# Optimization experiments

Measured on AMD Instinct MI355X. Metric: run time of the kernel, lower is better.

Reference implementation:

```python
import jax, jax.numpy as jnp
import numpy as np

NEG_SLOPE = 0.01  # torch F.leaky_relu default
NUM_USER, NUM_ITEM, DIM = 50000, 30000, 64
N_NODES = NUM_USER + NUM_ITEM
N_INTER = 800000
N_LAYERS = 2


def _leaky(x):
    return jax.nn.leaky_relu(x, NEG_SLOPE)


def _gcn_tower(features, preference, id_embedding, W, b, row, col):
    # x = cat(preference, features); F.normalize (L2 per row)
    x = jnp.concatenate([preference, features], axis=0)  # [N, 64]
    x = x / jnp.maximum(jnp.linalg.norm(x, axis=1, keepdims=True), 1e-12)
    deg = jax.ops.segment_sum(jnp.ones(row.shape, x.dtype), row, num_segments=N_NODES)  # bincount(row)
    for i in range(N_LAYERS):
        # Abstract_GCN: scatter-mean of gathered neighbor feats, then linear
        agg = jax.ops.segment_sum(x[col], row, num_segments=N_NODES) / deg[:, None]
        h = _leaky(agg @ W[i, 0].T + b[i, 0])
        # has_id=True, concate=False
        x_hat = _leaky(x @ W[i, 1].T + b[i, 1]) + id_embedding
        x = _leaky(h @ W[i, 2].T + b[i, 2] + x_hat)
    return x


def setup_inputs() -> dict:
    key = jax.random.key(0)
    ks = jax.random.split(key, 14)
    # bipartite user->item edges with full node coverage (every node appears
    # as a row after symmetrization, matching real interaction data where
    # bincount(row) has no zeros)
    r1 = jnp.arange(NUM_USER, dtype=jnp.int64 if jax.config.jax_enable_x64 else jnp.int32)
    c1 = jax.random.randint(ks[0], (NUM_USER,), NUM_USER, N_NODES)
    r2 = jax.random.randint(ks[1], (NUM_ITEM,), 0, NUM_USER)
    c2 = NUM_USER + jnp.arange(NUM_ITEM, dtype=r1.dtype)
    rest = N_INTER - NUM_USER - NUM_ITEM
    r3 = jax.random.randint(ks[2], (rest,), 0, NUM_USER)
    c3 = jax.random.randint(ks[3], (rest,), NUM_USER, N_NODES)
    row0 = jnp.concatenate([r1, r2, r3])
    col0 = jnp.concatenate([c1, c2, c3])
    # symmetrize: cat(edge_index, edge_index[[1,0]])
    edge_index = jnp.stack([jnp.concatenate([row0, col0]),
                            jnp.concatenate([col0, row0])])  # [2, 1.6M]
    s = 0.1  # xavier-ish scale for 64x64
    return {
        "v_feat": jax.random.normal(ks[4], (NUM_ITEM, DIM), jnp.float32),
        "t_feat": jax.random.normal(ks[5], (NUM_ITEM, DIM), jnp.float32),
        "id_embedding": jax.random.normal(ks[6], (N_NODES, DIM), jnp.float32) * s,
        "v_pref": jax.random.normal(ks[7], (NUM_USER, DIM), jnp.float32) * s,
        "t_pref": jax.random.normal(ks[8], (NUM_USER, DIM), jnp.float32) * s,
        "v_W": jax.random.normal(ks[9], (N_LAYERS, 3, DIM, DIM), jnp.float32) * s,
        "v_b": jnp.zeros((N_LAYERS, 3, DIM), jnp.float32),
        "t_W": jax.random.normal(ks[10], (N_LAYERS, 3, DIM, DIM), jnp.float32) * s,
        "t_b": jnp.zeros((N_LAYERS, 3, DIM), jnp.float32),
        "edge_index": edge_index,
    }


def reference(v_feat, t_feat, id_embedding, v_pref, t_pref, v_W, v_b, t_W, t_b, edge_index):
    row, col = edge_index[0], edge_index[1]
    rep_v = _gcn_tower(v_feat, v_pref, id_embedding, v_W, v_b, row, col)
    rep_t = _gcn_tower(t_feat, t_pref, id_embedding, t_W, t_b, row, col)
    return (rep_v + rep_t) / 2.0  # MMGCN.get_rep representation
```

## Files before the change

### kernel.cpp

```cpp
#include <hip/hip_runtime.h>
#include <hip/hip_bf16.h>

#define NUM_USER 50000
#define N_NODES  80000
#define DIM      64
#define NEG_SLOPE 0.01f

#define NB 313
#define BSHIFT 8
#define RMASK 255
#define CSHIFT 17
#define CMASK 0x1FFFF
#define CAP 10240

typedef __attribute__((ext_vector_type(8))) short short8;
typedef __attribute__((ext_vector_type(4))) float f32x4;

typedef unsigned short XT;

__device__ __forceinline__ float leaky(float v) {
    return v > 0.0f ? v : v * NEG_SLOPE;
}

__device__ __forceinline__ int load_idx(const void* ei, int is64, long long pos) {
    if (is64) return (int)((const long long*)ei)[pos];
    return ((const int*)ei)[pos];
}
__device__ __forceinline__ float load_f(const void* p, int isbf16, size_t i) {
    if (isbf16) return __bfloat162float(((const __hip_bfloat16*)p)[i]);
    return ((const float*)p)[i];
}

__device__ __forceinline__ unsigned short f2bf(float f) {
    unsigned u = __float_as_uint(f);
    u += 0x7fffu + ((u >> 16) & 1u);
    return (unsigned short)(u >> 16);
}

__device__ __forceinline__ void acc8(float* a, uint4 r) {
    a[0] += __uint_as_float(r.x << 16);
    a[1] += __uint_as_float(r.x & 0xffff0000u);
    a[2] += __uint_as_float(r.y << 16);
    a[3] += __uint_as_float(r.y & 0xffff0000u);
    a[4] += __uint_as_float(r.z << 16);
    a[5] += __uint_as_float(r.z & 0xffff0000u);
    a[6] += __uint_as_float(r.w << 16);
    a[7] += __uint_as_float(r.w & 0xffff0000u);
}

__global__ void detect_kernel(const unsigned int* __restrict__ feat_words,
                              const int* __restrict__ ei_words,
                              int* __restrict__ flags,
                              int* __restrict__ bucketCur) {
    int lane = threadIdx.x & 63;
    for (int i = lane; i < 320; i += 64) bucketCur[i] = 0;
    int orv = 0;
    for (int i = lane * 2 + 1; i < 1024; i += 128) orv |= ei_words[i];
    int hits = 0;
    for (int i = lane; i < 256; i += 64) {
        unsigned e = (feat_words[i] >> 7) & 0xFF;
        hits += (e == 126 || e == 127) ? 1 : 0;
    }
    #pragma unroll
    for (int d = 32; d > 0; d >>= 1) {
        orv  |= __shfl_xor(orv, d, 64);
        hits += __shfl_xor(hits, d, 64);
    }
    if (lane == 0 && blockIdx.x == 0) {
        flags[0] = (orv == 0) ? 1 : 0;
        flags[1] = (hits > 64) ? 1 : 0;
    }
}

__global__ __launch_bounds__(256) void megafuse_kernel(
        const void* __restrict__ ei, int E, int binBlocks, int initBlocks,
        const int* __restrict__ flags,
        int* __restrict__ bucketCur, unsigned int* __restrict__ recs,
        const void* __restrict__ vp, const void* __restrict__ tp,
        const void* __restrict__ vf, const void* __restrict__ tf,
        XT* __restrict__ xc,
        const void* __restrict__ vW, const void* __restrict__ tW,
        const void* __restrict__ vb, const void* __restrict__ tb,
        unsigned short* __restrict__ Wbf, float* __restrict__ bfp) {
    if ((int)blockIdx.x < binBlocks) {
        __shared__ int bloc[320];
        __shared__ int bres[320];
        int tid = threadIdx.x;
        for (int i = tid; i < 320; i += 256) bloc[i] = 0;
        __syncthreads();
        int is64 = flags[0];
        long long base = (long long)blockIdx.x * 2048;
        int bb[8], cc[8], lp[8], rl[8];
        #pragma unroll
        for (int it = 0; it < 8; ++it) {
            bb[it] = -1;
            long long e = base + it * 256 + tid;
            if (e < E) {
                int r = load_idx(ei, is64, e);
                int c = load_idx(ei, is64, (long long)E + e);
                if ((unsigned)r < N_NODES && (unsigned)c < N_NODES) {
                    int b = r >> BSHIFT;
                    bb[it] = b;
                    cc[it] = c;
                    rl[it] = r & RMASK;
                    lp[it] = atomicAdd(&bloc[b], 1);
                }
            }
        }
        __syncthreads();
        for (int i = tid; i < NB; i += 256) {
            int v = bloc[i];
            bres[i] = v ? atomicAdd(&bucketCur[i], v) : 0;
        }
        __syncthreads();
        #pragma unroll
        for (int it = 0; it < 8; ++it) {
            if (bb[it] >= 0) {
                int pos = bres[bb[it]] + lp[it];
                if (pos < CAP)
                    recs[(size_t)bb[it] * CAP + pos] =
                        ((unsigned)rl[it] << CSHIFT) | (unsigned)cc[it];
            }
        }
    } else if ((int)blockIdx.x < binBlocks + initBlocks) {
        int n = (blockIdx.x - binBlocks) * 4 + (threadIdx.x >> 6);
        if (n >= N_NODES) return;
        int lane = threadIdx.x & 63;
        int isb = flags[1];
        float a, b;
        if (n < NUM_USER) {
            a = load_f(vp, isb, (size_t)n * DIM + lane);
            b = load_f(tp, isb, (size_t)n * DIM + lane);
        } else {
            a = load_f(vf, isb, (size_t)(n - NUM_USER) * DIM + lane);
            b = load_f(tf, isb, (size_t)(n - NUM_USER) * DIM + lane);
        }
        float sa = a * a, sb = b * b;
        #pragma unroll
        for (int d = 32; d > 0; d >>= 1) {
            sa += __shfl_xor(sa, d, 64);
            sb += __shfl_xor(sb, d, 64);
        }
        float ra = 1.0f / fmaxf(sqrtf(sa), 1e-12f);
        float rb = 1.0f / fmaxf(sqrtf(sb), 1e-12f);
        xc[(size_t)n * 128 + lane]      = f2bf(a * ra);
        xc[(size_t)n * 128 + 64 + lane] = f2bf(b * rb);
    } else {
        int isb = flags[1];
        int j = (blockIdx.x - binBlocks - initBlocks) * 256 + threadIdx.x;
        if (j < 2 * 24576) {
            int tw = j / 24576, r = j % 24576;
            Wbf[j] = f2bf(load_f(tw ? tW : vW, isb, r));
        } else if (j < 2 * 24576 + 2 * 384) {
            int i2 = j - 2 * 24576;
            int tw = i2 / 384, r = i2 % 384;
            bfp[i2] = load_f(tw ? tb : vb, isb, r);
        }
    }
}

__global__ __launch_bounds__(1024) void bin2csr_kernel(
        const unsigned int* __restrict__ recs,
        const int* __restrict__ bucketCur,
        int* __restrict__ cnt, int* __restrict__ cur,
        int* __restrict__ csr) {
    __shared__ int rcnt[256];
    __shared__ int sc[256];
    __shared__ int lcur[256];
    int b = blockIdx.x;
    int t = threadIdx.x;
    int base = b * CAP;
    int count = bucketCur[b];
    if (count > CAP) count = CAP;

    if (t < 256) { rcnt[t] = 0; lcur[t] = 0; }
    __syncthreads();
    for (int i = t; i < count; i += 1024) {
        unsigned rec = recs[(size_t)base + i];
        atomicAdd(&rcnt[rec >> CSHIFT], 1);
    }
    __syncthreads();
    int v = (t < 256) ? rcnt[t] : 0;
    if (t < 256) sc[t] = v;
    __syncthreads();
    for (int d = 1; d < 256; d <<= 1) {
        int x = 0;
        if (t < 256) { x = sc[t]; if (t >= d) x += sc[t - d]; }
        __syncthreads();
        if (t < 256) sc[t] = x;
        __syncthreads();
    }
    if (t < 256) {
        int row = (b << BSHIFT) + t;
        if (row < N_NODES) {
            cnt[row] = v;
            cur[row] = base + sc[t];
        }
    }
    __syncthreads();
    for (int i = t; i < count; i += 1024) {
        unsigned rec = recs[(size_t)base + i];
        int rloc = rec >> CSHIFT;
        int c = rec & CMASK;
        int pos = base + (sc[rloc] - rcnt[rloc]) + atomicAdd(&lcur[rloc], 1);
        csr[pos] = c;
    }
}

__global__ __launch_bounds__(512) void gather_kernel(
        const XT* __restrict__ xc, XT* __restrict__ agg,
        const int* __restrict__ cnt, const int* __restrict__ cur,
        const int* __restrict__ csr) {
    int n = blockIdx.x * 8 + (threadIdx.x >> 6);
    if (n >= N_NODES) return;
    int lane = threadIdx.x & 63;
    int g8 = lane >> 3;
    int s  = lane & 7;
    int gg = g8 >> 1;
    int h  = g8 & 1;

    int d = cnt[n];
    int base = cur[n] - d;
    const int* nb = csr + base;
    const XT* xh = xc + h * 64;

    float acc[8];
    #pragma unroll
    for (int f = 0; f < 8; ++f) acc[f] = 0.f;

    int jj = gg;
    for (; jj + 4 < d; jj += 8) {
        int c0 = nb[jj];
        int c1 = nb[jj + 4];
        uint4 r0 = ((const uint4*)(xh + (size_t)c0 * 128))[s];
        uint4 r1 = ((const uint4*)(xh + (size_t)c1 * 128))[s];
        acc8(acc, r0);
        acc8(acc, r1);
    }
    if (jj < d) {
        int c0 = nb[jj];
        uint4 r0 = ((const uint4*)(xh + (size_t)c0 * 128))[s];
        acc8(acc, r0);
    }

    #pragma unroll
    for (int dd = 16; dd < 64; dd <<= 1) {
        #pragma unroll
        for (int f = 0; f < 8; ++f) acc[f] += __shfl_xor(acc[f], dd, 64);
    }

    float invd = (d > 0) ? 1.0f / (float)d : 0.0f;
    if (g8 < 2) {
        uint4 w;
        w.x = (unsigned)f2bf(acc[0] * invd) | ((unsigned)f2bf(acc[1] * invd) << 16);
        w.y = (unsigned)f2bf(acc[2] * invd) | ((unsigned)f2bf(acc[3] * invd) << 16);
        w.z = (unsigned)f2bf(acc[4] * invd) | ((unsigned)f2bf(acc[5] * invd) << 16);
        w.w = (unsigned)f2bf(acc[6] * invd) | ((unsigned)f2bf(acc[7] * invd) << 16);
        ((uint4*)(agg + (size_t)n * 128 + h * 64))[s] = w;
    }
}

__global__ __launch_bounds__(256) void dense_mfma_kernel(
        XT* __restrict__ xc, const XT* __restrict__ agg,
        void* __restrict__ out, int last,
        const void* __restrict__ id_emb,
        const unsigned short* __restrict__ Wbf, const float* __restrict__ bfp,
        int layer, const int* __restrict__ flags) {
    __shared__ unsigned short hts[4][16 * 72];
    __shared__ float res[2][16][65];
    int wave = threadIdx.x >> 6, lane = threadIdx.x & 63;
    int quad = lane >> 4, l16 = lane & 15;
    int tile  = wave >> 1;
    int tower = wave & 1;
    int isb = flags[1];
    int n0 = (blockIdx.x * 2 + tile) * 16;
    int toff = tower * 64;
    const unsigned short* Wm = Wbf + (size_t)((tower * 2 + layer) * 3) * 4096;
    const float* bb = bfp + (tower * 2 + layer) * 192;
    unsigned short* ht = hts[wave];

    size_t arow = (size_t)(n0 + l16) * 128 + toff + quad * 8;

    short8 x0  = *(const short8*)(xc + arow);
    short8 x1  = *(const short8*)(xc + arow + 32);
    short8 ga0 = *(const short8*)(agg + arow);
    short8 ga1 = *(const short8*)(agg + arow + 32);

    f32x4 accP[4];

    #pragma unroll
    for (int t = 0; t < 4; ++t) {
        f32x4 c = {0.f, 0.f, 0.f, 0.f};
        short8 b0 = *(const short8*)(Wm + 4096 + (16 * t + l16) * 64 + quad * 8);
        short8 b1 = *(const short8*)(Wm + 4096 + (16 * t + l16) * 64 + 32 + quad * 8);
        c = __builtin_amdgcn_mfma_f32_16x16x32_bf16(x0, b0, c, 0, 0, 0);
        c = __builtin_amdgcn_mfma_f32_16x16x32_bf16(x1, b1, c, 0, 0, 0);
        float bias = bb[64 + 16 * t + l16];
        #pragma unroll
        for (int r = 0; r < 4; ++r) accP[t][r] = leaky(c[r] + bias);
    }

    #pragma unroll
    for (int t = 0; t < 4; ++t) {
        f32x4 c = {0.f, 0.f, 0.f, 0.f};
        short8 b0 = *(const short8*)(Wm + (16 * t + l16) * 64 + quad * 8);
        short8 b1 = *(const short8*)(Wm + (16 * t + l16) * 64 + 32 + quad * 8);
        c = __builtin_amdgcn_mfma_f32_16x16x32_bf16(ga0, b0, c, 0, 0, 0);
        c = __builtin_amdgcn_mfma_f32_16x16x32_bf16(ga1, b1, c, 0, 0, 0);
        float bias = bb[16 * t + l16];
        #pragma unroll
        for (int r = 0; r < 4; ++r)
            ht[(quad * 4 + r) * 72 + 16 * t + l16] = f2bf(leaky(c[r] + bias));
    }

    float idv[16];
    #pragma unroll
    for (int t = 0; t < 4; ++t)
        #pragma unroll
        for (int r = 0; r < 4; ++r)
            idv[t * 4 + r] = load_f(id_emb, isb,
                                    (size_t)(n0 + quad * 4 + r) * 64 + 16 * t + l16);

    short8 a0 = *(const short8*)(ht + l16 * 72 + quad * 8);
    short8 a1 = *(const short8*)(ht + l16 * 72 + 32 + quad * 8);

    float xres[16];
    #pragma unroll
    for (int t = 0; t < 4; ++t) {
        f32x4 c = {0.f, 0.f, 0.f, 0.f};
        short8 b0 = *(const short8*)(Wm + 2 * 4096 + (16 * t + l16) * 64 + quad * 8);
        short8 b1 = *(const short8*)(Wm + 2 * 4096 + (16 * t + l16) * 64 + 32 + quad * 8);
        c = __builtin_amdgcn_mfma_f32_16x16x32_bf16(a0, b0, c, 0, 0, 0);
        c = __builtin_amdgcn_mfma_f32_16x16x32_bf16(a1, b1, c, 0, 0, 0);
        float bias = bb[128 + 16 * t + l16];
        #pragma unroll
        for (int r = 0; r < 4; ++r)
            xres[t * 4 + r] = leaky(c[r] + bias + accP[t][r] + idv[t * 4 + r]);
    }

    if (!last) {
        #pragma unroll
        for (int t = 0; t < 4; ++t) {
            #pragma unroll
            for (int r = 0; r < 4; ++r) {
                int node2 = n0 + quad * 4 + r;
                int j = 16 * t + l16;
                xc[(size_t)node2 * 128 + toff + j] = f2bf(xres[t * 4 + r]);
            }
        }
    } else {
        if (tower == 1) {
            #pragma unroll
            for (int t = 0; t < 4; ++t)
                #pragma unroll
                for (int r = 0; r < 4; ++r)
                    res[tile][quad * 4 + r][16 * t + l16] = xres[t * 4 + r];
        }
        __syncthreads();
        if (tower == 0) {
            #pragma unroll
            for (int t = 0; t < 4; ++t) {
                #pragma unroll
                for (int r = 0; r < 4; ++r) {
                    int node2 = n0 + quad * 4 + r;
                    int j = 16 * t + l16;
                    float avg = (xres[t * 4 + r] + res[tile][quad * 4 + r][j]) * 0.5f;
                    if (isb) ((unsigned short*)out)[(size_t)node2 * 64 + j] = f2bf(avg);
                    else     ((float*)out)[(size_t)node2 * 64 + j] = avg;
                }
            }
        }
    }
}

extern "C" void kernel_launch(void* const* d_in, const int* in_sizes, int n_in,
                              void* d_out, int out_size, void* d_ws, size_t ws_size,
                              hipStream_t stream) {
    const void* v_feat = d_in[0];
    const void* t_feat = d_in[1];
    const void* id_emb = d_in[2];
    const void* v_pref = d_in[3];
    const void* t_pref = d_in[4];
    const void* v_W    = d_in[5];
    const void* v_b    = d_in[6];
    const void* t_W    = d_in[7];
    const void* t_b    = d_in[8];
    const void* ei     = d_in[9];

    const int E = in_sizes[9] / 2;
    char* ws = (char*)d_ws;

    size_t o = 0;
    int*            flags     = (int*)(ws + o);            o += 16;
    int*            cnt       = (int*)(ws + o);            o += 320000;
    int*            cur       = (int*)(ws + o);            o += 320000;
    int*            bucketCur = (int*)(ws + o);            o += 320 * 4;
    unsigned short* Wbf       = (unsigned short*)(ws + o); o += 2 * 24576 * 2;
    float*          bfp       = (float*)(ws + o);          o += 2 * 384 * 4;
    XT* xc  = (XT*)(ws + o); o += (size_t)N_NODES * 128 * sizeof(XT);
    XT* agg = (XT*)(ws + o); o += (size_t)N_NODES * 128 * sizeof(XT);
    unsigned int* recs = (unsigned int*)(ws + o); o += (size_t)NB * CAP * 4;
    int* csr = (int*)(ws + o);

    detect_kernel<<<dim3(1), dim3(64), 0, stream>>>(
        (const unsigned int*)v_feat, (const int*)ei, flags, bucketCur);

    const int binBlocks  = (E + 2047) / 2048;
    const int initBlocks = (N_NODES + 3) / 4;
    const int packBlocks = (2 * 24576 + 2 * 384 + 255) / 256;
    megafuse_kernel<<<dim3(binBlocks + initBlocks + packBlocks), dim3(256), 0, stream>>>(
        ei, E, binBlocks, initBlocks, flags, bucketCur, recs,
        v_pref, t_pref, v_feat, t_feat, xc,
        v_W, t_W, v_b, t_b, Wbf, bfp);

    bin2csr_kernel<<<dim3(NB), dim3(1024), 0, stream>>>(recs, bucketCur, cnt, cur, csr);

    const int gatherBlocks = (N_NODES + 7) / 8;
    const int denseBlocks  = N_NODES / 32;

    gather_kernel<<<dim3(gatherBlocks), dim3(512), 0, stream>>>(xc, agg, cnt, cur, csr);
    dense_mfma_kernel<<<dim3(denseBlocks), dim3(256), 0, stream>>>(
        xc, agg, d_out, 0, id_emb, Wbf, bfp, 0, flags);
    gather_kernel<<<dim3(gatherBlocks), dim3(512), 0, stream>>>(xc, agg, cnt, cur, csr);
    dense_mfma_kernel<<<dim3(denseBlocks), dim3(256), 0, stream>>>(
        xc, agg, d_out, 1, id_emb, Wbf, bfp, 1, flags);
}
```

Baseline: 365.5 us.

## Stage dense-layer weights in LDS and split towers across grid y

The dense MFMA kernel now copies the three 64x64 bf16 weight matrices for its tower into padded shared memory once per block, and the MFMA B operands are read from there instead of from global memory. Blocks grow to 8 waves, each handling a 16-node tile of a single tower chosen by blockIdx.y. The final tower averaging moves out of the last dense kernel into a separate elementwise kernel that reads both bf16 tower outputs. This aims to cut repeated global weight loads, at the cost of an extra kernel launch, an extra pass over xc, and rounding the last layer to bf16 before averaging.

After: 344.6 us (median of 2 runs). 5.7% less time.

```diff
diff --git a/kernel.cpp b/kernel.cpp
--- a/kernel.cpp
+++ b/kernel.cpp
@@ -260,25 +260,32 @@
     }
 }
 
-__global__ __launch_bounds__(256) void dense_mfma_kernel(
+__global__ __launch_bounds__(512) void dense_mfma_kernel(
         XT* __restrict__ xc, const XT* __restrict__ agg,
-        void* __restrict__ out, int last,
         const void* __restrict__ id_emb,
         const unsigned short* __restrict__ Wbf, const float* __restrict__ bfp,
         int layer, const int* __restrict__ flags) {
-    __shared__ unsigned short hts[4][16 * 72];
-    __shared__ float res[2][16][65];
+    __shared__ unsigned short Wl[3 * 64 * 72];
+    __shared__ unsigned short hts[8][16 * 72];
+    int tower = blockIdx.y;
     int wave = threadIdx.x >> 6, lane = threadIdx.x & 63;
     int quad = lane >> 4, l16 = lane & 15;
-    int tile  = wave >> 1;
-    int tower = wave & 1;
     int isb = flags[1];
-    int n0 = (blockIdx.x * 2 + tile) * 16;
     int toff = tower * 64;
-    const unsigned short* Wm = Wbf + (size_t)((tower * 2 + layer) * 3) * 4096;
+    const unsigned short* Wg = Wbf + (size_t)((tower * 2 + layer) * 3) * 4096;
     const float* bb = bfp + (tower * 2 + layer) * 192;
     unsigned short* ht = hts[wave];
 
+    for (int i = threadIdx.x; i < 1536; i += 512) {
+        int lin = i * 8;
+        int mat = lin >> 12;
+        int rem = lin & 4095;
+        uint4 v = *(const uint4*)(Wg + lin);
+        *(uint4*)(Wl + mat * 4608 + (rem >> 6) * 72 + (rem & 63)) = v;
+    }
+    __syncthreads();
+
+    int n0 = (blockIdx.x * 8 + wave) * 16;
     size_t arow = (size_t)(n0 + l16) * 128 + toff + quad * 8;
 
     short8 x0  = *(const short8*)(xc + arow);
@@ -291,8 +298,8 @@
     #pragma unroll
     for (int t = 0; t < 4; ++t) {
         f32x4 c = {0.f, 0.f, 0.f, 0.f};
-        short8 b0 = *(const short8*)(Wm + 4096 + (16 * t + l16) * 64 + quad * 8);
-        short8 b1 = *(const short8*)(Wm + 4096 + (16 * t + l16) * 64 + 32 + quad * 8);
+        short8 b0 = *(const short8*)(Wl + 4608 + (16 * t + l16) * 72 + quad * 8);
+        short8 b1 = *(const short8*)(Wl + 4608 + (16 * t + l16) * 72 + 32 + quad * 8);
         c = __builtin_amdgcn_mfma_f32_16x16x32_bf16(x0, b0, c, 0, 0, 0);
         c = __builtin_amdgcn_mfma_f32_16x16x32_bf16(x1, b1, c, 0, 0, 0);
         float bias = bb[64 + 16 * t + l16];
@@ -303,8 +310,8 @@
     #pragma unroll
     for (int t = 0; t < 4; ++t) {
         f32x4 c = {0.f, 0.f, 0.f, 0.f};
-        short8 b0 = *(const short8*)(Wm + (16 * t + l16) * 64 + quad * 8);
-        short8 b1 = *(const short8*)(Wm + (16 * t + l16) * 64 + 32 + quad * 8);
+        short8 b0 = *(const short8*)(Wl + (16 * t + l16) * 72 + quad * 8);
+        short8 b1 = *(const short8*)(Wl + (16 * t + l16) * 72 + 32 + quad * 8);
         c = __builtin_amdgcn_mfma_f32_16x16x32_bf16(ga0, b0, c, 0, 0, 0);
         c = __builtin_amdgcn_mfma_f32_16x16x32_bf16(ga1, b1, c, 0, 0, 0);
         float bias = bb[16 * t + l16];
@@ -324,52 +331,51 @@
     short8 a0 = *(const short8*)(ht + l16 * 72 + quad * 8);
     short8 a1 = *(const short8*)(ht + l16 * 72 + 32 + quad * 8);
 
-    float xres[16];
     #pragma unroll
     for (int t = 0; t < 4; ++t) {
         f32x4 c = {0.f, 0.f, 0.f, 0.f};
-        short8 b0 = *(const short8*)(Wm + 2 * 4096 + (16 * t + l16) * 64 + quad * 8);
-        short8 b1 = *(const short8*)(Wm + 2 * 4096 + (16 * t + l16) * 64 + 32 + quad * 8);
+        short8 b0 = *(const short8*)(Wl + 2 * 4608 + (16 * t + l16) * 72 + quad * 8);
+        short8 b1 = *(const short8*)(Wl + 2 * 4608 + (16 * t + l16) * 72 + 32 + quad * 8);
         c = __builtin_amdgcn_mfma_f32_16x16x32_bf16(a0, b0, c, 0, 0, 0);
         c = __builtin_amdgcn_mfma_f32_16x16x32_bf16(a1, b1, c, 0, 0, 0);
         float bias = bb[128 + 16 * t + l16];
         #pragma unroll
-        for (int r = 0; r < 4; ++r)
-            xres[t * 4 + r] = leaky(c[r] + bias + accP[t][r] + idv[t * 4 + r]);
-    }
-
-    if (!last) {
-        #pragma unroll
-        for (int t = 0; t < 4; ++t) {
-            #pragma unroll
-            for (int r = 0; r < 4; ++r) {
-                int node2 = n0 + quad * 4 + r;
-                int j = 16 * t + l16;
-                xc[(size_t)node2 * 128 + toff + j] = f2bf(xres[t * 4 + r]);
-            }
-        }
+        for (int r = 0; r < 4; ++r) {
+            int node2 = n0 + quad * 4 + r;
+            int j = 16 * t + l16;
+            float v = leaky(c[r] + bias + accP[t][r] + idv[t * 4 + r]);
+            xc[(size_t)node2 * 128 + toff + j] = f2bf(v);
+        }
+    }
+}
+
+__global__ void final_kernel(const XT* __restrict__ xc, void* __restrict__ out,
+                             const int* __restrict__ flags, int n8) {
+    int i = blockIdx.x * blockDim.x + threadIdx.x;
+    if (i >= n8) return;
+    int n = i >> 3, s = i & 7;
+    uint4 v = ((const uint4*)(xc + (size_t)n * 128))[s];
+    uint4 t = ((const uint4*)(xc + (size_t)n * 128 + 64))[s];
+    float r[8];
+    r[0] = (__uint_as_float(v.x << 16) + __uint_as_float(t.x << 16)) * 0.5f;
+    r[1] = (__uint_as_float(v.x & 0xffff0000u) + __uint_as_float(t.x & 0xffff0000u)) * 0.5f;
+    r[2] = (__uint_as_float(v.y << 16) + __uint_as_float(t.y << 16)) * 0.5f;
+    r[3] = (__uint_as_float(v.y & 0xffff0000u) + __uint_as_float(t.y & 0xffff0000u)) * 0.5f;
+    r[4] = (__uint_as_float(v.z << 16) + __uint_as_float(t.z << 16)) * 0.5f;
+    r[5] = (__uint_as_float(v.z & 0xffff0000u) + __uint_as_float(t.z & 0xffff0000u)) * 0.5f;
+    r[6] = (__uint_as_float(v.w << 16) + __uint_as_float(t.w << 16)) * 0.5f;
+    r[7] = (__uint_as_float(v.w & 0xffff0000u) + __uint_as_float(t.w & 0xffff0000u)) * 0.5f;
+    if (flags[1]) {
+        uint4 o;
+        o.x = (unsigned)f2bf(r[0]) | ((unsigned)f2bf(r[1]) << 16);
+        o.y = (unsigned)f2bf(r[2]) | ((unsigned)f2bf(r[3]) << 16);
+        o.z = (unsigned)f2bf(r[4]) | ((unsigned)f2bf(r[5]) << 16);
+        o.w = (unsigned)f2bf(r[6]) | ((unsigned)f2bf(r[7]) << 16);
+        ((uint4*)out)[i] = o;
     } else {
-        if (tower == 1) {
-            #pragma unroll
-            for (int t = 0; t < 4; ++t)
-                #pragma unroll
-                for (int r = 0; r < 4; ++r)
-                    res[tile][quad * 4 + r][16 * t + l16] = xres[t * 4 + r];
-        }
-        __syncthreads();
-        if (tower == 0) {
-            #pragma unroll
-            for (int t = 0; t < 4; ++t) {
-                #pragma unroll
-                for (int r = 0; r < 4; ++r) {
-                    int node2 = n0 + quad * 4 + r;
-                    int j = 16 * t + l16;
-                    float avg = (xres[t * 4 + r] + res[tile][quad * 4 + r][j]) * 0.5f;
-                    if (isb) ((unsigned short*)out)[(size_t)node2 * 64 + j] = f2bf(avg);
-                    else     ((float*)out)[(size_t)node2 * 64 + j] = avg;
-                }
-            }
-        }
+        float4* o = (float4*)out;
+        o[i * 2 + 0] = make_float4(r[0], r[1], r[2], r[3]);
+        o[i * 2 + 1] = make_float4(r[4], r[5], r[6], r[7]);
     }
 }
 
@@ -416,12 +422,14 @@
     bin2csr_kernel<<<dim3(NB), dim3(1024), 0, stream>>>(recs, bucketCur, cnt, cur, csr);
 
     const int gatherBlocks = (N_NODES + 7) / 8;
-    const int denseBlocks  = N_NODES / 32;
-
-    gather_kernel<<<dim3(gatherBlocks), dim3(512), 0, stream>>>(xc, agg, cnt, cur, csr);
-    dense_mfma_kernel<<<dim3(denseBlocks), dim3(256), 0, stream>>>(
-        xc, agg, d_out, 0, id_emb, Wbf, bfp, 0, flags);
-    gather_kernel<<<dim3(gatherBlocks), dim3(512), 0, stream>>>(xc, agg, cnt, cur, csr);
-    dense_mfma_kernel<<<dim3(denseBlocks), dim3(256), 0, stream>>>(
-        xc, agg, d_out, 1, id_emb, Wbf, bfp, 1, flags);
-}
+    const int denseBlocksX = N_NODES / (16 * 8);
+
+    for (int layer = 0; layer < 2; ++layer) {
+        gather_kernel<<<dim3(gatherBlocks), dim3(512), 0, stream>>>(xc, agg, cnt, cur, csr);
+        dense_mfma_kernel<<<dim3(denseBlocksX, 2), dim3(512), 0, stream>>>(
+            xc, agg, id_emb, Wbf, bfp, layer, flags);
+    }
+
+    const int n8 = N_NODES * DIM / 8;
+    final_kernel<<<dim3((n8 + 255) / 256), dim3(256), 0, stream>>>(xc, d_out, flags, n8);
+}
```
